# Optimization experiments

Measured on AMD Instinct MI355X. Metric: run time of the kernel, lower is better.

## Reference

```python
import jax, jax.numpy as jnp
import numpy as np

INPUT_DIM = 512
OUTPUT_DIM = 512
DEGREE = 7
ALPHA = 0.5


def setup_inputs() -> dict:
    key = jax.random.key(0)
    kx, kc = jax.random.split(key)
    x = jax.random.normal(kx, (8192, INPUT_DIM), dtype=jnp.float32)
    std = 1.0 / (INPUT_DIM * (DEGREE + 1))
    laguerre_coeffs = jax.random.normal(kc, (INPUT_DIM, OUTPUT_DIM, DEGREE + 1), dtype=jnp.float32) * std
    return {"x": x, "laguerre_coeffs": laguerre_coeffs}


def reference(x, laguerre_coeffs):
    # x: [B, I] -> tanh squashed
    xt = jnp.tanh(x.reshape(-1, INPUT_DIM))
    # Build Laguerre basis L_0..L_degree via the standard recurrence:
    # k*L_k = (2(k-1)+1+alpha - x)*L_{k-1} - (k-1+alpha)*L_{k-2}
    L0 = jnp.ones_like(xt)
    basis = [L0]
    if DEGREE > 0:
        L1 = 1.0 + ALPHA - xt
        basis.append(L1)
        Lkm2, Lkm1 = L0, L1
        for k in range(2, DEGREE + 1):
            Lk = ((2 * (k - 1) + 1 + ALPHA - xt) * Lkm1 - (k - 1 + ALPHA) * Lkm2) / k
            basis.append(Lk)
            Lkm2, Lkm1 = Lkm1, Lk
    laguerre = jnp.stack(basis, axis=-1)  # [B, I, D+1]
    y = jnp.einsum('bid,iod->bo', laguerre, laguerre_coeffs)
    return y
```

## Files before the change

### kernel.cpp

```cpp
#include <hip/hip_runtime.h>

#define B_ROWS 8192
#define IN_DIM 512
#define OUT_DIM 512
#define NDEG 8
#define KDIM (IN_DIM * NDEG)
#define ZSLICES 4
#define NKT 16

typedef short bf16x8 __attribute__((ext_vector_type(8)));
typedef float f32x4  __attribute__((ext_vector_type(4)));

__device__ __forceinline__ unsigned short f2bf(float f) {
  unsigned u = __float_as_uint(f);
  u += 0x7fffu + ((u >> 16) & 1u);
  return (unsigned short)(u >> 16);
}

__device__ __forceinline__ void laguerre8(float t, float* L) {
  L[0] = 1.0f;
  L[1] = 1.5f - t;
#pragma unroll
  for (int k = 2; k < NDEG; ++k)
    L[k] = ((2.0f * (float)k - 0.5f - t) * L[k - 1] -
            ((float)k - 0.5f) * L[k - 2]) * (1.0f / (float)k);
}


__global__ void prep_kernel(const float* __restrict__ x, const float* __restrict__ cf,
                            unsigned short* __restrict__ A, unsigned short* __restrict__ Bt) {
  int g = blockIdx.x;
  if (g < (B_ROWS * IN_DIM) / 256) {
    int idx = g * 256 + threadIdx.x;
    int b = idx >> 9, i = idx & 511;
    float L[NDEG];
    laguerre8(tanhf(x[idx]), L);
    uint4 v;
    v.x = (unsigned)f2bf(L[0]) | ((unsigned)f2bf(L[1]) << 16);
    v.y = (unsigned)f2bf(L[2]) | ((unsigned)f2bf(L[3]) << 16);
    v.z = (unsigned)f2bf(L[4]) | ((unsigned)f2bf(L[5]) << 16);
    v.w = (unsigned)f2bf(L[6]) | ((unsigned)f2bf(L[7]) << 16);
    int h = b >> 7, rb = b & 127, t = i >> 3, c = i & 7;
    size_t chunk = ((size_t)(h * 64 + t)) * 1024 + (rb >> 6) * 512 + (rb & 63) * 8 + (c ^ (rb & 7));
    ((uint4*)A)[chunk] = v;
  } else {
    int idx = (g - (B_ROWS * IN_DIM) / 256) * 256 + threadIdx.x;
    int i = idx >> 9, o = idx & 511;
    const float4* cp = (const float4*)(cf + (size_t)idx * 8);
    float4 c0 = cp[0], c1 = cp[1];
    uint4 v;
    v.x = (unsigned)f2bf(c0.x) | ((unsigned)f2bf(c0.y) << 16);
    v.y = (unsigned)f2bf(c0.z) | ((unsigned)f2bf(c0.w) << 16);
    v.z = (unsigned)f2bf(c1.x) | ((unsigned)f2bf(c1.y) << 16);
    v.w = (unsigned)f2bf(c1.z) | ((unsigned)f2bf(c1.w) << 16);
    int h = o >> 7, rb = o & 127, t = i >> 3, c = i & 7;
    size_t chunk = ((size_t)(h * 64 + t)) * 1024 + (rb >> 6) * 512 + (rb & 63) * 8 + (c ^ (rb & 7));
    ((uint4*)Bt)[chunk] = v;
  }
}

__global__ __launch_bounds__(512, 2) void gemm_kernel(const unsigned short* __restrict__ A,
                                                      const unsigned short* __restrict__ Bt,
                                                      unsigned short* __restrict__ P) {
  __shared__ unsigned short lds[65536];

  const int tid = threadIdx.x;
  const int lane = tid & 63;
  const int w = tid >> 6;
  const int wm = w >> 2, wn = w & 3;

  const int g = blockIdx.x;
  const int j0 = g >> 3, xx = g & 7;
  const int My = ((j0 >> 3) << 3) | xx;
  const int n = (j0 >> 2) & 1;
  const int z = j0 & 3;

  const uint4* Ag = (const uint4*)A;
  const uint4* Bg = (const uint4*)Bt;

  const int arow = lane & 15, hi = lane >> 4;
  const int e0 = (hi ^ (arow & 7)) * 8;

  f32x4 zero = {0.f, 0.f, 0.f, 0.f};
  f32x4 acc[8][4];
#pragma unroll
  for (int mi = 0; mi < 8; ++mi)
#pragma unroll
    for (int ni = 0; ni < 4; ++ni) acc[mi][ni] = zero;

  auto STAGE = [&](int tile, int buf) {
    const int tg = z * NKT + tile;
    const size_t cA0 = ((size_t)((My * 2 + 0) * 64 + tg)) * 1024 + w * 64 + lane;
    const size_t cA1 = ((size_t)((My * 2 + 1) * 64 + tg)) * 1024 + w * 64 + lane;
    const size_t cB0 = ((size_t)((n * 2 + 0) * 64 + tg)) * 1024 + w * 64 + lane;
    const size_t cB1 = ((size_t)((n * 2 + 1) * 64 + tg)) * 1024 + w * 64 + lane;
    unsigned short* dA = lds + buf * 16384 + w * 512;
    unsigned short* dB = lds + 32768 + buf * 16384 + w * 512;
#pragma unroll
    for (int j = 0; j < 2; ++j) {
      __builtin_amdgcn_global_load_lds(
          (const __attribute__((address_space(1))) unsigned int*)(Ag + cA0 + j * 512),
          (__attribute__((address_space(3))) unsigned int*)(dA + j * 4096), 16, 0, 0);
      __builtin_amdgcn_global_load_lds(
          (const __attribute__((address_space(1))) unsigned int*)(Ag + cA1 + j * 512),
          (__attribute__((address_space(3))) unsigned int*)(dA + 8192 + j * 4096), 16, 0, 0);
      __builtin_amdgcn_global_load_lds(
          (const __attribute__((address_space(1))) unsigned int*)(Bg + cB0 + j * 512),
          (__attribute__((address_space(3))) unsigned int*)(dB + j * 4096), 16, 0, 0);
      __builtin_amdgcn_global_load_lds(
          (const __attribute__((address_space(1))) unsigned int*)(Bg + cB1 + j * 512),
          (__attribute__((address_space(3))) unsigned int*)(dB + 8192 + j * 4096), 16, 0, 0);
    }
  };

  auto COMPUTE = [&](int buf) {
    const unsigned short* Ab = lds + buf * 16384 + wm * 8192;
    const unsigned short* Bb = lds + 32768 + buf * 16384 + (wn >> 1) * 8192 + (wn & 1) * 4096;
#pragma unroll
    for (int ks = 0; ks < 2; ++ks) {
      bf16x8 af[8], bfr[4];
#pragma unroll
      for (int mi = 0; mi < 8; ++mi)
        af[mi] = *(const bf16x8*)(Ab + (mi >> 2) * 4096 + ((mi & 3) * 16 + arow) * 64 + (e0 ^ (ks * 32)));
#pragma unroll
      for (int ni = 0; ni < 4; ++ni)
        bfr[ni] = *(const bf16x8*)(Bb + (ni * 16 + arow) * 64 + (e0 ^ (ks * 32)));
      __builtin_amdgcn_s_setprio(1);
#pragma unroll
      for (int mi = 0; mi < 8; ++mi)
#pragma unroll
        for (int ni = 0; ni < 4; ++ni)
          acc[mi][ni] = __builtin_amdgcn_mfma_f32_16x16x32_bf16(af[mi], bfr[ni], acc[mi][ni], 0, 0, 0);
      __builtin_amdgcn_s_setprio(0);
    }
  };

  STAGE(0, 0);
  STAGE(1, 1);
  asm volatile("s_waitcnt vmcnt(8)" ::: "memory");
  __builtin_amdgcn_sched_barrier(0);
  __builtin_amdgcn_s_barrier();

  for (int t = 0; t < NKT - 2; ++t) {
    const int cur = t & 1;
    COMPUTE(cur);
    asm volatile("s_waitcnt lgkmcnt(0)" ::: "memory");
    __builtin_amdgcn_sched_barrier(0);
    __builtin_amdgcn_s_barrier();
    STAGE(t + 2, cur);
    asm volatile("s_waitcnt vmcnt(8)" ::: "memory");
    __builtin_amdgcn_sched_barrier(0);
    __builtin_amdgcn_s_barrier();
  }
  COMPUTE(0);
  asm volatile("s_waitcnt vmcnt(0)" ::: "memory");
  __builtin_amdgcn_sched_barrier(0);
  __builtin_amdgcn_s_barrier();
  COMPUTE(1);
  __syncthreads();

  unsigned short* W = lds + w * 8192;
#pragma unroll
  for (int mi = 0; mi < 8; ++mi)
#pragma unroll
    for (int ni = 0; ni < 4; ++ni) {
      int col = ni * 16 + arow;
      int c8 = col >> 3, cpos = col & 7;
#pragma unroll
      for (int r = 0; r < 4; ++r) {
        int row = mi * 16 + hi * 4 + r;
        W[row * 64 + ((c8 ^ (row & 7)) << 3) + cpos] = f2bf(acc[mi][ni][r]);
      }
    }
  const int rr = lane >> 3, cc = lane & 7;
#pragma unroll
  for (int it = 0; it < 16; ++it) {
    int row = it * 8 + rr;
    uint4 v = *(uint4*)&W[row * 64 + ((cc ^ (row & 7)) << 3)];
    size_t pr = ((size_t)z * B_ROWS + My * 256 + wm * 128 + row) * 512 + n * 256 + wn * 64 + cc * 8;
    *(uint4*)&P[pr] = v;
  }
}

__global__ void reduce_kernel(const unsigned short* __restrict__ P, float* __restrict__ out) {
  size_t t = (size_t)blockIdx.x * 256 + threadIdx.x;
  const uint4* p = (const uint4*)P;
  const size_t stride = (size_t)B_ROWS * OUT_DIM / 8;
  float s[8] = {0, 0, 0, 0, 0, 0, 0, 0};
#pragma unroll
  for (int zz = 0; zz < ZSLICES; ++zz) {
    uint4 v = p[t + zz * stride];
    unsigned q[4] = {v.x, v.y, v.z, v.w};
#pragma unroll
    for (int j = 0; j < 4; ++j) {
      s[2 * j]     += __uint_as_float((q[j] & 0xffffu) << 16);
      s[2 * j + 1] += __uint_as_float(q[j] & 0xffff0000u);
    }
  }
  float4 o0 = {s[0], s[1], s[2], s[3]}, o1 = {s[4], s[5], s[6], s[7]};
  ((float4*)out)[t * 2]     = o0;
  ((float4*)out)[t * 2 + 1] = o1;
}

__global__ void naive_kernel(const float* __restrict__ x, const float* __restrict__ c,
                             float* __restrict__ out) {
  __shared__ float bas[IN_DIM * NDEG];
  int b = blockIdx.x;
  for (int i = threadIdx.x; i < IN_DIM; i += 256) {
    float t = tanhf(x[(size_t)b * IN_DIM + i]);
    float L[NDEG];
    laguerre8(t, L);
#pragma unroll
    for (int d = 0; d < NDEG; ++d) bas[i * NDEG + d] = L[d];
  }
  __syncthreads();
  for (int o = threadIdx.x; o < OUT_DIM; o += 256) {
    float acc = 0.f;
    for (int i = 0; i < IN_DIM; ++i) {
      const float* cp = c + ((size_t)i * OUT_DIM + o) * NDEG;
#pragma unroll
      for (int d = 0; d < NDEG; ++d) acc += bas[i * NDEG + d] * cp[d];
    }
    out[(size_t)b * OUT_DIM + o] = acc;
  }
}

extern "C" void kernel_launch(void* const* d_in, const int* in_sizes, int n_in,
                              void* d_out, int out_size, void* d_ws, size_t ws_size,
                              hipStream_t stream) {
  const float* x    = (const float*)d_in[0];
  const float* coef = (const float*)d_in[1];
  float* out = (float*)d_out;

  const size_t A_BYTES  = (size_t)B_ROWS * KDIM * 2;
  const size_t P_BYTES  = (size_t)ZSLICES * B_ROWS * OUT_DIM * 2;
  const size_t BT_BYTES = (size_t)OUT_DIM * KDIM * 2;

  if (ws_size >= A_BYTES + P_BYTES + BT_BYTES) {
    unsigned short* Abuf = (unsigned short*)d_ws;
    unsigned short* Pp   = (unsigned short*)((char*)d_ws + A_BYTES);
    unsigned short* Bt   = (unsigned short*)((char*)d_ws + A_BYTES + P_BYTES);
    prep_kernel<<<(B_ROWS * IN_DIM + IN_DIM * OUT_DIM) / 256, 256, 0, stream>>>(x, coef, Abuf, Bt);
    gemm_kernel<<<256, 512, 0, stream>>>(Abuf, Bt, Pp);
    reduce_kernel<<<(B_ROWS * OUT_DIM / 8) / 256, 256, 0, stream>>>(Pp, out);
  } else {
    naive_kernel<<<B_ROWS, 256, 0, stream>>>(x, coef, out);
  }
}
```

Before: 67.95 us.

## Interleave half-tile async loads with MFMA phases in fine-grained GEMM pipeline

Replaces the per-tile compute-then-stage double-buffer loop with eight phases per tile pair, each issuing one half-tile global-to-LDS load and running a quarter of the MFMA work, with barriers and vmcnt waits placed between phases. Fragment registers shrink to 4 A and 4 B vectors. The aim is to spread memory traffic across compute so loads overlap MFMA execution more evenly and register pressure drops. The cost is many more barriers per tile and tighter ordering assumptions about which buffer halves are safe to overwrite.

```diff
diff --git a/kernel.cpp b/kernel.cpp
--- a/kernel.cpp
+++ b/kernel.cpp
@@ -59,6 +59,35 @@
   }
 }
 
+
+#define PH(buf, mq, ks, LOADBF, VMW, ...)                                          \
+  {                                                                                \
+    const unsigned short* Ab_ = lds + (buf)*16384 + wm*8192 + (mq)*4096 + arow*64; \
+    _Pragma("unroll") for (int m4 = 0; m4 < 4; ++m4)                               \
+      af[m4] = *(const bf16x8*)(Ab_ + m4*1024 + (e ^ ((ks)*32)));                  \
+    if (LOADBF) {                                                                  \
+      const unsigned short* Bb_ = lds + 32768 + (buf)*16384 + (wn>>1)*8192         \
+                                  + (wn&1)*4096 + arow*64;                         \
+      _Pragma("unroll") for (int ni = 0; ni < 4; ++ni)                             \
+        bfr[ni] = *(const bf16x8*)(Bb_ + ni*1024 + (e ^ ((ks)*32)));               \
+    }                                                                              \
+    __VA_ARGS__;                                                                   \
+    __builtin_amdgcn_s_barrier();                                                  \
+    asm volatile("s_waitcnt lgkmcnt(0)" ::: "memory");                             \
+    __builtin_amdgcn_sched_barrier(0);                                             \
+    __builtin_amdgcn_s_setprio(1);                                                 \
+    _Pragma("unroll") for (int m4 = 0; m4 < 4; ++m4)                               \
+      _Pragma("unroll") for (int ni = 0; ni < 4; ++ni)                             \
+        acc[(mq)*4+m4][ni] = __builtin_amdgcn_mfma_f32_16x16x32_bf16(              \
+            af[m4], bfr[ni], acc[(mq)*4+m4][ni], 0, 0, 0);                         \
+    __builtin_amdgcn_s_setprio(0);                                                 \
+    if ((VMW) == 1) { asm volatile("s_waitcnt vmcnt(2)" ::: "memory");             \
+                      __builtin_amdgcn_sched_barrier(0); }                         \
+    if ((VMW) == 2) { asm volatile("s_waitcnt vmcnt(0)" ::: "memory");             \
+                      __builtin_amdgcn_sched_barrier(0); }                         \
+    __builtin_amdgcn_s_barrier();                                                  \
+  }
+
 __global__ __launch_bounds__(512, 2) void gemm_kernel(const unsigned short* __restrict__ A,
                                                       const unsigned short* __restrict__ Bt,
                                                       unsigned short* __restrict__ P) {
@@ -79,7 +108,7 @@
   const uint4* Bg = (const uint4*)Bt;
 
   const int arow = lane & 15, hi = lane >> 4;
-  const int e0 = (hi ^ (arow & 7)) * 8;
+  const int e = (hi ^ (arow & 7)) * 8;
 
   f32x4 zero = {0.f, 0.f, 0.f, 0.f};
   f32x4 acc[8][4];
@@ -88,76 +117,47 @@
 #pragma unroll
     for (int ni = 0; ni < 4; ++ni) acc[mi][ni] = zero;
 
-  auto STAGE = [&](int tile, int buf) {
-    const int tg = z * NKT + tile;
-    const size_t cA0 = ((size_t)((My * 2 + 0) * 64 + tg)) * 1024 + w * 64 + lane;
-    const size_t cA1 = ((size_t)((My * 2 + 1) * 64 + tg)) * 1024 + w * 64 + lane;
-    const size_t cB0 = ((size_t)((n * 2 + 0) * 64 + tg)) * 1024 + w * 64 + lane;
-    const size_t cB1 = ((size_t)((n * 2 + 1) * 64 + tg)) * 1024 + w * 64 + lane;
-    unsigned short* dA = lds + buf * 16384 + w * 512;
-    unsigned short* dB = lds + 32768 + buf * 16384 + w * 512;
-#pragma unroll
-    for (int j = 0; j < 2; ++j) {
-      __builtin_amdgcn_global_load_lds(
-          (const __attribute__((address_space(1))) unsigned int*)(Ag + cA0 + j * 512),
-          (__attribute__((address_space(3))) unsigned int*)(dA + j * 4096), 16, 0, 0);
-      __builtin_amdgcn_global_load_lds(
-          (const __attribute__((address_space(1))) unsigned int*)(Ag + cA1 + j * 512),
-          (__attribute__((address_space(3))) unsigned int*)(dA + 8192 + j * 4096), 16, 0, 0);
-      __builtin_amdgcn_global_load_lds(
-          (const __attribute__((address_space(1))) unsigned int*)(Bg + cB0 + j * 512),
-          (__attribute__((address_space(3))) unsigned int*)(dB + j * 4096), 16, 0, 0);
-      __builtin_amdgcn_global_load_lds(
-          (const __attribute__((address_space(1))) unsigned int*)(Bg + cB1 + j * 512),
-          (__attribute__((address_space(3))) unsigned int*)(dB + 8192 + j * 4096), 16, 0, 0);
-    }
+  auto STAGE_H = [&](int isB, int h, int tile, int buf) {
+    const uint4* src = isB ? Bg : Ag;
+    const int rowblk = (isB ? n * 2 : My * 2) + h;
+    const size_t c0 = ((size_t)(rowblk * 64 + z * NKT + tile)) * 1024 + w * 64 + lane;
+    unsigned short* d = lds + isB * 32768 + buf * 16384 + h * 8192 + w * 512;
+    __builtin_amdgcn_global_load_lds(
+        (const __attribute__((address_space(1))) unsigned int*)(src + c0),
+        (__attribute__((address_space(3))) unsigned int*)d, 16, 0, 0);
+    __builtin_amdgcn_global_load_lds(
+        (const __attribute__((address_space(1))) unsigned int*)(src + c0 + 512),
+        (__attribute__((address_space(3))) unsigned int*)(d + 4096), 16, 0, 0);
   };
 
-  auto COMPUTE = [&](int buf) {
-    const unsigned short* Ab = lds + buf * 16384 + wm * 8192;
-    const unsigned short* Bb = lds + 32768 + buf * 16384 + (wn >> 1) * 8192 + (wn & 1) * 4096;
-#pragma unroll
-    for (int ks = 0; ks < 2; ++ks) {
-      bf16x8 af[8], bfr[4];
-#pragma unroll
-      for (int mi = 0; mi < 8; ++mi)
-        af[mi] = *(const bf16x8*)(Ab + (mi >> 2) * 4096 + ((mi & 3) * 16 + arow) * 64 + (e0 ^ (ks * 32)));
-#pragma unroll
-      for (int ni = 0; ni < 4; ++ni)
-        bfr[ni] = *(const bf16x8*)(Bb + (ni * 16 + arow) * 64 + (e0 ^ (ks * 32)));
-      __builtin_amdgcn_s_setprio(1);
-#pragma unroll
-      for (int mi = 0; mi < 8; ++mi)
-#pragma unroll
-        for (int ni = 0; ni < 4; ++ni)
-          acc[mi][ni] = __builtin_amdgcn_mfma_f32_16x16x32_bf16(af[mi], bfr[ni], acc[mi][ni], 0, 0, 0);
-      __builtin_amdgcn_s_setprio(0);
-    }
-  };
-
-  STAGE(0, 0);
-  STAGE(1, 1);
-  asm volatile("s_waitcnt vmcnt(8)" ::: "memory");
+  bf16x8 af[4], bfr[4];
+
+  STAGE_H(0, 0, 0, 0); STAGE_H(0, 1, 0, 0);
+  STAGE_H(1, 0, 0, 0); STAGE_H(1, 1, 0, 0);
+  STAGE_H(1, 0, 1, 1);
+  asm volatile("s_waitcnt vmcnt(2)" ::: "memory");
   __builtin_amdgcn_sched_barrier(0);
   __builtin_amdgcn_s_barrier();
 
-  for (int t = 0; t < NKT - 2; ++t) {
-    const int cur = t & 1;
-    COMPUTE(cur);
-    asm volatile("s_waitcnt lgkmcnt(0)" ::: "memory");
-    __builtin_amdgcn_sched_barrier(0);
-    __builtin_amdgcn_s_barrier();
-    STAGE(t + 2, cur);
-    asm volatile("s_waitcnt vmcnt(8)" ::: "memory");
-    __builtin_amdgcn_sched_barrier(0);
-    __builtin_amdgcn_s_barrier();
-  }
-  COMPUTE(0);
-  asm volatile("s_waitcnt vmcnt(0)" ::: "memory");
-  __builtin_amdgcn_sched_barrier(0);
-  __builtin_amdgcn_s_barrier();
-  COMPUTE(1);
-  __syncthreads();
+  for (int it = 0; it < 7; ++it) {
+    const int t1 = 2 * it + 1, t2 = 2 * it + 2, t3 = 2 * it + 3;
+    PH(0, 0, 0, 1, 0, STAGE_H(1, 1, t1, 1));
+    PH(0, 1, 0, 0, 0, STAGE_H(0, 0, t1, 1));
+    PH(0, 0, 1, 1, 0, STAGE_H(0, 1, t1, 1));
+    PH(0, 1, 1, 0, 1, STAGE_H(1, 0, t2, 0));
+    PH(1, 0, 0, 1, 0, STAGE_H(0, 0, t2, 0));
+    PH(1, 1, 0, 0, 0, STAGE_H(0, 1, t2, 0));
+    PH(1, 0, 1, 1, 0, STAGE_H(1, 1, t2, 0));
+    PH(1, 1, 1, 0, 1, STAGE_H(1, 0, t3, 1));
+  }
+  PH(0, 0, 0, 1, 0, STAGE_H(1, 1, 15, 1));
+  PH(0, 1, 0, 0, 0, STAGE_H(0, 0, 15, 1));
+  PH(0, 0, 1, 1, 0, STAGE_H(0, 1, 15, 1));
+  PH(0, 1, 1, 0, 2, (void)0);
+  PH(1, 0, 0, 1, 0, (void)0);
+  PH(1, 1, 0, 0, 0, (void)0);
+  PH(1, 0, 1, 1, 0, (void)0);
+  PH(1, 1, 1, 0, 0, (void)0);
 
   unsigned short* W = lds + w * 8192;
 #pragma unroll
```

New measurement: 67.10 us. About the same (-1.2%).

## Fuse split-K reduction into GEMM via atomic counters and shrink tiles

Applied to the files above, without the earlier changes.

Tiles shrink from 256x256 to 128x128 with split-K reduced from 4 to 2 slices, so 512 blocks run with 4 blocks per CU and smaller LDS. The separate reduce kernel is removed: the last block per output tile, found with an atomic counter, sums the two bf16 partials into the output. The prep kernel now writes contiguous swizzled A chunks with coalesced stores and uses a fast exp-based tanh. This cuts one kernel launch and halves partial-sum traffic, at the cost of a memset, atomics and lower per-block reuse.

```diff
diff --git a/kernel.cpp b/kernel.cpp
--- a/kernel.cpp
+++ b/kernel.cpp
@@ -5,8 +5,8 @@
 #define OUT_DIM 512
 #define NDEG 8
 #define KDIM (IN_DIM * NDEG)
-#define ZSLICES 4
-#define NKT 16
+#define ZS 2
+#define NKT 32
 
 typedef short bf16x8 __attribute__((ext_vector_type(8)));
 typedef float f32x4  __attribute__((ext_vector_type(4)));
@@ -26,25 +26,39 @@
             ((float)k - 0.5f) * L[k - 2]) * (1.0f / (float)k);
 }
 
+__device__ __forceinline__ float ftanh(float x) {
+  float e2 = __expf(2.0f * x);
+  return (e2 - 1.0f) * (1.0f / (e2 + 1.0f));
+}
+
+__device__ __forceinline__ uint4 bpack(float xv) {
+  float L[NDEG];
+  laguerre8(ftanh(xv), L);
+  uint4 v;
+  v.x = (unsigned)f2bf(L[0]) | ((unsigned)f2bf(L[1]) << 16);
+  v.y = (unsigned)f2bf(L[2]) | ((unsigned)f2bf(L[3]) << 16);
+  v.z = (unsigned)f2bf(L[4]) | ((unsigned)f2bf(L[5]) << 16);
+  v.w = (unsigned)f2bf(L[6]) | ((unsigned)f2bf(L[7]) << 16);
+  return v;
+}
+
 
 __global__ void prep_kernel(const float* __restrict__ x, const float* __restrict__ cf,
                             unsigned short* __restrict__ A, unsigned short* __restrict__ Bt) {
-  int g = blockIdx.x;
-  if (g < (B_ROWS * IN_DIM) / 256) {
-    int idx = g * 256 + threadIdx.x;
-    int b = idx >> 9, i = idx & 511;
-    float L[NDEG];
-    laguerre8(tanhf(x[idx]), L);
-    uint4 v;
-    v.x = (unsigned)f2bf(L[0]) | ((unsigned)f2bf(L[1]) << 16);
-    v.y = (unsigned)f2bf(L[2]) | ((unsigned)f2bf(L[3]) << 16);
-    v.z = (unsigned)f2bf(L[4]) | ((unsigned)f2bf(L[5]) << 16);
-    v.w = (unsigned)f2bf(L[6]) | ((unsigned)f2bf(L[7]) << 16);
-    int h = b >> 7, rb = b & 127, t = i >> 3, c = i & 7;
-    size_t chunk = ((size_t)(h * 64 + t)) * 1024 + (rb >> 6) * 512 + (rb & 63) * 8 + (c ^ (rb & 7));
-    ((uint4*)A)[chunk] = v;
+  const int g = blockIdx.x, tid = threadIdx.x;
+  if (g < 4096) {
+    const int h = g >> 6, t = g & 63;
+    uint4* dst = (uint4*)A + (size_t)g * 1024;
+#pragma unroll
+    for (int q = 0; q < 4; ++q) {
+      int v = q * 256 + tid;
+      int rb = ((v >> 9) << 6) | ((v >> 3) & 63);
+      int c = (v & 7) ^ (rb & 7);
+      float xv = x[(size_t)(h * 128 + rb) * 512 + t * 8 + c];
+      dst[v] = bpack(xv);
+    }
   } else {
-    int idx = (g - (B_ROWS * IN_DIM) / 256) * 256 + threadIdx.x;
+    int idx = (g - 4096) * 256 + tid;
     int i = idx >> 9, o = idx & 511;
     const float4* cp = (const float4*)(cf + (size_t)idx * 8);
     float4 c0 = cp[0], c1 = cp[1];
@@ -59,10 +73,21 @@
   }
 }
 
-__global__ __launch_bounds__(512, 2) void gemm_kernel(const unsigned short* __restrict__ A,
+
+#define VM(N) { asm volatile("s_waitcnt vmcnt(" #N ")" ::: "memory");  \
+                __builtin_amdgcn_sched_barrier(0); }
+#define GL16(s, d)                                                      \
+  __builtin_amdgcn_global_load_lds(                                     \
+      (const __attribute__((address_space(1))) unsigned int*)(s),       \
+      (__attribute__((address_space(3))) unsigned int*)(d), 16, 0, 0)
+
+__global__ __launch_bounds__(512, 4) void gemm_kernel(const unsigned short* __restrict__ A,
                                                       const unsigned short* __restrict__ Bt,
-                                                      unsigned short* __restrict__ P) {
-  __shared__ unsigned short lds[65536];
+                                                      unsigned short* __restrict__ P,
+                                                      float* __restrict__ out,
+                                                      unsigned int* __restrict__ cnt) {
+  __shared__ __align__(16) unsigned short lds[32768];
+  __shared__ int lastFlag;
 
   const int tid = threadIdx.x;
   const int lane = tid & 63;
@@ -70,77 +95,61 @@
   const int wm = w >> 2, wn = w & 3;
 
   const int g = blockIdx.x;
-  const int j0 = g >> 3, xx = g & 7;
-  const int My = ((j0 >> 3) << 3) | xx;
-  const int n = (j0 >> 2) & 1;
-  const int z = j0 & 3;
+  const int slot = g >> 3, xcd = g & 7;
+  const int My = ((slot & 7) << 3) | xcd;
+  const int n = (slot >> 3) & 3;
+  const int z = slot >> 5;
 
   const uint4* Ag = (const uint4*)A;
   const uint4* Bg = (const uint4*)Bt;
 
   const int arow = lane & 15, hi = lane >> 4;
-  const int e0 = (hi ^ (arow & 7)) * 8;
+  const int e = (hi ^ (arow & 7)) * 8;
 
   f32x4 zero = {0.f, 0.f, 0.f, 0.f};
-  f32x4 acc[8][4];
-#pragma unroll
-  for (int mi = 0; mi < 8; ++mi)
-#pragma unroll
-    for (int ni = 0; ni < 4; ++ni) acc[mi][ni] = zero;
-
-  auto STAGE = [&](int tile, int buf) {
-    const int tg = z * NKT + tile;
-    const size_t cA0 = ((size_t)((My * 2 + 0) * 64 + tg)) * 1024 + w * 64 + lane;
-    const size_t cA1 = ((size_t)((My * 2 + 1) * 64 + tg)) * 1024 + w * 64 + lane;
-    const size_t cB0 = ((size_t)((n * 2 + 0) * 64 + tg)) * 1024 + w * 64 + lane;
-    const size_t cB1 = ((size_t)((n * 2 + 1) * 64 + tg)) * 1024 + w * 64 + lane;
-    unsigned short* dA = lds + buf * 16384 + w * 512;
-    unsigned short* dB = lds + 32768 + buf * 16384 + w * 512;
-#pragma unroll
-    for (int j = 0; j < 2; ++j) {
-      __builtin_amdgcn_global_load_lds(
-          (const __attribute__((address_space(1))) unsigned int*)(Ag + cA0 + j * 512),
-          (__attribute__((address_space(3))) unsigned int*)(dA + j * 4096), 16, 0, 0);
-      __builtin_amdgcn_global_load_lds(
-          (const __attribute__((address_space(1))) unsigned int*)(Ag + cA1 + j * 512),
-          (__attribute__((address_space(3))) unsigned int*)(dA + 8192 + j * 4096), 16, 0, 0);
-      __builtin_amdgcn_global_load_lds(
-          (const __attribute__((address_space(1))) unsigned int*)(Bg + cB0 + j * 512),
-          (__attribute__((address_space(3))) unsigned int*)(dB + j * 4096), 16, 0, 0);
-      __builtin_amdgcn_global_load_lds(
-          (const __attribute__((address_space(1))) unsigned int*)(Bg + cB1 + j * 512),
-          (__attribute__((address_space(3))) unsigned int*)(dB + 8192 + j * 4096), 16, 0, 0);
-    }
+  f32x4 acc[4][2];
+#pragma unroll
+  for (int m4 = 0; m4 < 4; ++m4)
+#pragma unroll
+    for (int ni = 0; ni < 2; ++ni) acc[m4][ni] = zero;
+
+  auto STAGE = [&](int t, int buf) {
+    const int tg = z * NKT + t;
+    const uint4* a = Ag + ((size_t)(My * 64 + tg)) * 1024 + w * 128 + lane;
+    unsigned short* dA = lds + buf * 8192 + w * 1024;
+    GL16(a, dA); GL16(a + 64, dA + 512);
+    const uint4* b = Bg + ((size_t)(n * 64 + tg)) * 1024 + w * 128 + lane;
+    unsigned short* dB = lds + 16384 + buf * 8192 + w * 1024;
+    GL16(b, dB); GL16(b + 64, dB + 512);
   };
 
   auto COMPUTE = [&](int buf) {
-    const unsigned short* Ab = lds + buf * 16384 + wm * 8192;
-    const unsigned short* Bb = lds + 32768 + buf * 16384 + (wn >> 1) * 8192 + (wn & 1) * 4096;
+    const unsigned short* Ab = lds + buf * 8192 + wm * 4096 + arow * 64;
+    const unsigned short* Bb = lds + 16384 + buf * 8192 + (wn >> 1) * 4096
+                               + (wn & 1) * 2048 + arow * 64;
 #pragma unroll
     for (int ks = 0; ks < 2; ++ks) {
-      bf16x8 af[8], bfr[4];
-#pragma unroll
-      for (int mi = 0; mi < 8; ++mi)
-        af[mi] = *(const bf16x8*)(Ab + (mi >> 2) * 4096 + ((mi & 3) * 16 + arow) * 64 + (e0 ^ (ks * 32)));
-#pragma unroll
-      for (int ni = 0; ni < 4; ++ni)
-        bfr[ni] = *(const bf16x8*)(Bb + (ni * 16 + arow) * 64 + (e0 ^ (ks * 32)));
+      const int o = e ^ (ks * 32);
+      bf16x8 af[4], bfr[2];
+#pragma unroll
+      for (int m4 = 0; m4 < 4; ++m4) af[m4] = *(const bf16x8*)(Ab + m4 * 1024 + o);
+#pragma unroll
+      for (int ni = 0; ni < 2; ++ni) bfr[ni] = *(const bf16x8*)(Bb + ni * 1024 + o);
       __builtin_amdgcn_s_setprio(1);
 #pragma unroll
-      for (int mi = 0; mi < 8; ++mi)
-#pragma unroll
-        for (int ni = 0; ni < 4; ++ni)
-          acc[mi][ni] = __builtin_amdgcn_mfma_f32_16x16x32_bf16(af[mi], bfr[ni], acc[mi][ni], 0, 0, 0);
+      for (int m4 = 0; m4 < 4; ++m4)
+#pragma unroll
+        for (int ni = 0; ni < 2; ++ni)
+          acc[m4][ni] = __builtin_amdgcn_mfma_f32_16x16x32_bf16(af[m4], bfr[ni], acc[m4][ni], 0, 0, 0);
       __builtin_amdgcn_s_setprio(0);
     }
   };
 
-  STAGE(0, 0);
-  STAGE(1, 1);
-  asm volatile("s_waitcnt vmcnt(8)" ::: "memory");
-  __builtin_amdgcn_sched_barrier(0);
+  STAGE(0, 0); STAGE(1, 1);
+  VM(4);
   __builtin_amdgcn_s_barrier();
 
+#pragma unroll 2
   for (int t = 0; t < NKT - 2; ++t) {
     const int cur = t & 1;
     COMPUTE(cur);
@@ -148,58 +157,65 @@
     __builtin_amdgcn_sched_barrier(0);
     __builtin_amdgcn_s_barrier();
     STAGE(t + 2, cur);
-    asm volatile("s_waitcnt vmcnt(8)" ::: "memory");
-    __builtin_amdgcn_sched_barrier(0);
+    VM(4);
     __builtin_amdgcn_s_barrier();
   }
   COMPUTE(0);
-  asm volatile("s_waitcnt vmcnt(0)" ::: "memory");
-  __builtin_amdgcn_sched_barrier(0);
+  VM(0);
   __builtin_amdgcn_s_barrier();
   COMPUTE(1);
   __syncthreads();
 
-  unsigned short* W = lds + w * 8192;
-#pragma unroll
-  for (int mi = 0; mi < 8; ++mi)
-#pragma unroll
-    for (int ni = 0; ni < 4; ++ni) {
+  unsigned short* W = lds + w * 4096;
+#pragma unroll
+  for (int m4 = 0; m4 < 4; ++m4)
+#pragma unroll
+    for (int ni = 0; ni < 2; ++ni) {
       int col = ni * 16 + arow;
       int c8 = col >> 3, cpos = col & 7;
 #pragma unroll
       for (int r = 0; r < 4; ++r) {
-        int row = mi * 16 + hi * 4 + r;
-        W[row * 64 + ((c8 ^ (row & 7)) << 3) + cpos] = f2bf(acc[mi][ni][r]);
+        int row = m4 * 16 + hi * 4 + r;
+        W[row * 64 + ((c8 ^ (row & 7)) << 3) + cpos] = f2bf(acc[m4][ni][r]);
       }
     }
-  const int rr = lane >> 3, cc = lane & 7;
-#pragma unroll
-  for (int it = 0; it < 16; ++it) {
-    int row = it * 8 + rr;
-    uint4 v = *(uint4*)&W[row * 64 + ((cc ^ (row & 7)) << 3)];
-    size_t pr = ((size_t)z * B_ROWS + My * 256 + wm * 128 + row) * 512 + n * 256 + wn * 64 + cc * 8;
+#pragma unroll
+  for (int it = 0; it < 4; ++it) {
+    int row = it * 16 + (lane >> 2), cc2 = lane & 3;
+    uint4 v = *(uint4*)&W[row * 64 + ((cc2 ^ (row & 7)) << 3)];
+    size_t pr = (size_t)z * ((size_t)B_ROWS * OUT_DIM)
+              + (size_t)(My * 128 + wm * 64 + row) * 512 + n * 128 + wn * 32 + cc2 * 8;
     *(uint4*)&P[pr] = v;
   }
-}
-
-__global__ void reduce_kernel(const unsigned short* __restrict__ P, float* __restrict__ out) {
-  size_t t = (size_t)blockIdx.x * 256 + threadIdx.x;
-  const uint4* p = (const uint4*)P;
-  const size_t stride = (size_t)B_ROWS * OUT_DIM / 8;
-  float s[8] = {0, 0, 0, 0, 0, 0, 0, 0};
-#pragma unroll
-  for (int zz = 0; zz < ZSLICES; ++zz) {
-    uint4 v = p[t + zz * stride];
-    unsigned q[4] = {v.x, v.y, v.z, v.w};
-#pragma unroll
-    for (int j = 0; j < 4; ++j) {
-      s[2 * j]     += __uint_as_float((q[j] & 0xffffu) << 16);
-      s[2 * j + 1] += __uint_as_float(q[j] & 0xffff0000u);
-    }
-  }
-  float4 o0 = {s[0], s[1], s[2], s[3]}, o1 = {s[4], s[5], s[6], s[7]};
-  ((float4*)out)[t * 2]     = o0;
-  ((float4*)out)[t * 2 + 1] = o1;
+
+  __threadfence();
+  if (tid == 0)
+    lastFlag = (atomicAdd(&cnt[My * 4 + n], 1u) == 1u);
+  __syncthreads();
+  if (lastFlag) {
+    __threadfence();
+    const size_t ss = (size_t)B_ROWS * OUT_DIM;
+#pragma unroll
+    for (int q = 0; q < 4; ++q) {
+      int el = q * 512 + tid;
+      int row = el >> 4, cc = el & 15;
+      size_t off = (size_t)(My * 128 + row) * 512 + n * 128 + cc * 8;
+      uint4 a = *(const uint4*)&P[off];
+      uint4 b = *(const uint4*)&P[off + ss];
+      unsigned qa[4] = {a.x, a.y, a.z, a.w}, qb[4] = {b.x, b.y, b.z, b.w};
+      float s[8];
+#pragma unroll
+      for (int j = 0; j < 4; ++j) {
+        s[2 * j]     = __uint_as_float((qa[j] & 0xffffu) << 16) +
+                       __uint_as_float((qb[j] & 0xffffu) << 16);
+        s[2 * j + 1] = __uint_as_float(qa[j] & 0xffff0000u) +
+                       __uint_as_float(qb[j] & 0xffff0000u);
+      }
+      float4 f0 = {s[0], s[1], s[2], s[3]}, f1 = {s[4], s[5], s[6], s[7]};
+      *(float4*)&out[off]     = f0;
+      *(float4*)&out[off + 4] = f1;
+    }
+  }
 }
 
 __global__ void naive_kernel(const float* __restrict__ x, const float* __restrict__ c,
@@ -232,17 +248,19 @@
   const float* coef = (const float*)d_in[1];
   float* out = (float*)d_out;
 
-  const size_t A_BYTES  = (size_t)B_ROWS * KDIM * 2;
-  const size_t P_BYTES  = (size_t)ZSLICES * B_ROWS * OUT_DIM * 2;
-  const size_t BT_BYTES = (size_t)OUT_DIM * KDIM * 2;
-
-  if (ws_size >= A_BYTES + P_BYTES + BT_BYTES) {
+  const size_t A_B   = (size_t)B_ROWS * KDIM * 2;
+  const size_t P_B   = (size_t)ZS * B_ROWS * OUT_DIM * 2;
+  const size_t BT_B  = (size_t)OUT_DIM * KDIM * 2;
+  const size_t CNT_B = 1024;
+
+  if (ws_size >= A_B + P_B + BT_B + CNT_B) {
     unsigned short* Abuf = (unsigned short*)d_ws;
-    unsigned short* Pp   = (unsigned short*)((char*)d_ws + A_BYTES);
-    unsigned short* Bt   = (unsigned short*)((char*)d_ws + A_BYTES + P_BYTES);
-    prep_kernel<<<(B_ROWS * IN_DIM + IN_DIM * OUT_DIM) / 256, 256, 0, stream>>>(x, coef, Abuf, Bt);
-    gemm_kernel<<<256, 512, 0, stream>>>(Abuf, Bt, Pp);
-    reduce_kernel<<<(B_ROWS * OUT_DIM / 8) / 256, 256, 0, stream>>>(Pp, out);
+    unsigned short* Pp   = (unsigned short*)((char*)d_ws + A_B);
+    unsigned short* Bt   = (unsigned short*)((char*)d_ws + A_B + P_B);
+    unsigned int*   cnt  = (unsigned int*)((char*)d_ws + A_B + P_B + BT_B);
+    hipMemsetAsync(cnt, 0, CNT_B, stream);
+    prep_kernel<<<4096 + 1024, 256, 0, stream>>>(x, coef, Abuf, Bt);
+    gemm_kernel<<<512, 512, 0, stream>>>(Abuf, Bt, Pp, out, cnt);
   } else {
     naive_kernel<<<B_ROWS, 256, 0, stream>>>(x, coef, out);
   }
```

Result: slower. 239.6 us (+252.6%).

## Shrink GEMM tiles to 128x128, halve split-K slices, use fast tanh

Applied to the files above, without the earlier changes.

The GEMM block tile goes from 256x256 with 8 waves to 128x128 with 4 waves, and the launch goes from 256 to 512 blocks. Split-K drops from 4 slices to 2, so each block runs 32 K-tiles and the partial buffer and reduce traffic are halved. The prep kernel swaps tanhf for an exp-based fast tanh, which is cheaper but could overflow for large inputs. Smaller tiles mean less data reuse per block and more global traffic for A and B, in exchange for fewer partial sums and possibly better occupancy; s_setprio is also dropped.

```diff
diff --git a/kernel.cpp b/kernel.cpp
--- a/kernel.cpp
+++ b/kernel.cpp
@@ -5,11 +5,13 @@
 #define OUT_DIM 512
 #define NDEG 8
 #define KDIM (IN_DIM * NDEG)
-#define ZSLICES 4
-#define NKT 16
+#define ZS 2
+#define NKT 32
 
 typedef short bf16x8 __attribute__((ext_vector_type(8)));
 typedef float f32x4  __attribute__((ext_vector_type(4)));
+
+#define SB __builtin_amdgcn_sched_barrier(0)
 
 __device__ __forceinline__ unsigned short f2bf(float f) {
   unsigned u = __float_as_uint(f);
@@ -24,6 +26,22 @@
   for (int k = 2; k < NDEG; ++k)
     L[k] = ((2.0f * (float)k - 0.5f - t) * L[k - 1] -
             ((float)k - 0.5f) * L[k - 2]) * (1.0f / (float)k);
+}
+
+__device__ __forceinline__ float ftanh(float x) {
+  float e2 = __expf(2.0f * x);
+  return (e2 - 1.0f) * (1.0f / (e2 + 1.0f));
+}
+
+__device__ __forceinline__ uint4 bpack(float xv) {
+  float L[NDEG];
+  laguerre8(ftanh(xv), L);
+  uint4 v;
+  v.x = (unsigned)f2bf(L[0]) | ((unsigned)f2bf(L[1]) << 16);
+  v.y = (unsigned)f2bf(L[2]) | ((unsigned)f2bf(L[3]) << 16);
+  v.z = (unsigned)f2bf(L[4]) | ((unsigned)f2bf(L[5]) << 16);
+  v.w = (unsigned)f2bf(L[6]) | ((unsigned)f2bf(L[7]) << 16);
+  return v;
 }
 
 
@@ -33,13 +51,7 @@
   if (g < (B_ROWS * IN_DIM) / 256) {
     int idx = g * 256 + threadIdx.x;
     int b = idx >> 9, i = idx & 511;
-    float L[NDEG];
-    laguerre8(tanhf(x[idx]), L);
-    uint4 v;
-    v.x = (unsigned)f2bf(L[0]) | ((unsigned)f2bf(L[1]) << 16);
-    v.y = (unsigned)f2bf(L[2]) | ((unsigned)f2bf(L[3]) << 16);
-    v.z = (unsigned)f2bf(L[4]) | ((unsigned)f2bf(L[5]) << 16);
-    v.w = (unsigned)f2bf(L[6]) | ((unsigned)f2bf(L[7]) << 16);
+    uint4 v = bpack(x[idx]);
     int h = b >> 7, rb = b & 127, t = i >> 3, c = i & 7;
     size_t chunk = ((size_t)(h * 64 + t)) * 1024 + (rb >> 6) * 512 + (rb & 63) * 8 + (c ^ (rb & 7));
     ((uint4*)A)[chunk] = v;
@@ -59,109 +71,97 @@
   }
 }
 
-__global__ __launch_bounds__(512, 2) void gemm_kernel(const unsigned short* __restrict__ A,
+__global__ __launch_bounds__(256, 2) void gemm_kernel(const unsigned short* __restrict__ A,
                                                       const unsigned short* __restrict__ Bt,
                                                       unsigned short* __restrict__ P) {
-  __shared__ unsigned short lds[65536];
+  __shared__ unsigned short lds[32768];
 
   const int tid = threadIdx.x;
   const int lane = tid & 63;
   const int w = tid >> 6;
-  const int wm = w >> 2, wn = w & 3;
+  const int wm = w >> 1, wn = w & 1;
 
   const int g = blockIdx.x;
-  const int j0 = g >> 3, xx = g & 7;
-  const int My = ((j0 >> 3) << 3) | xx;
-  const int n = (j0 >> 2) & 1;
-  const int z = j0 & 3;
+  const int xx = g & 7, hy = (g >> 3) & 7;
+  const int My = hy * 8 + xx;
+  const int n = (g >> 6) & 3;
+  const int z = (g >> 8) & 1;
 
   const uint4* Ag = (const uint4*)A;
   const uint4* Bg = (const uint4*)Bt;
 
   const int arow = lane & 15, hi = lane >> 4;
-  const int e0 = (hi ^ (arow & 7)) * 8;
+  const int e = (hi ^ (arow & 7)) * 8;
 
   f32x4 zero = {0.f, 0.f, 0.f, 0.f};
-  f32x4 acc[8][4];
-#pragma unroll
-  for (int mi = 0; mi < 8; ++mi)
+  f32x4 acc[4][4];
+#pragma unroll
+  for (int mi = 0; mi < 4; ++mi)
 #pragma unroll
     for (int ni = 0; ni < 4; ++ni) acc[mi][ni] = zero;
 
   auto STAGE = [&](int tile, int buf) {
     const int tg = z * NKT + tile;
-    const size_t cA0 = ((size_t)((My * 2 + 0) * 64 + tg)) * 1024 + w * 64 + lane;
-    const size_t cA1 = ((size_t)((My * 2 + 1) * 64 + tg)) * 1024 + w * 64 + lane;
-    const size_t cB0 = ((size_t)((n * 2 + 0) * 64 + tg)) * 1024 + w * 64 + lane;
-    const size_t cB1 = ((size_t)((n * 2 + 1) * 64 + tg)) * 1024 + w * 64 + lane;
-    unsigned short* dA = lds + buf * 16384 + w * 512;
-    unsigned short* dB = lds + 32768 + buf * 16384 + w * 512;
-#pragma unroll
-    for (int j = 0; j < 2; ++j) {
+    const size_t cA = ((size_t)(My * 64 + tg)) * 1024 + w * 256 + lane;
+    const size_t cB = ((size_t)(n * 64 + tg)) * 1024 + w * 256 + lane;
+    unsigned short* dA = lds + buf * 8192 + w * 2048;
+    unsigned short* dB = lds + 16384 + buf * 8192 + w * 2048;
+#pragma unroll
+    for (int j = 0; j < 4; ++j) {
       __builtin_amdgcn_global_load_lds(
-          (const __attribute__((address_space(1))) unsigned int*)(Ag + cA0 + j * 512),
-          (__attribute__((address_space(3))) unsigned int*)(dA + j * 4096), 16, 0, 0);
+          (const __attribute__((address_space(1))) unsigned int*)(Ag + cA + j * 64),
+          (__attribute__((address_space(3))) unsigned int*)(dA + j * 512), 16, 0, 0);
       __builtin_amdgcn_global_load_lds(
-          (const __attribute__((address_space(1))) unsigned int*)(Ag + cA1 + j * 512),
-          (__attribute__((address_space(3))) unsigned int*)(dA + 8192 + j * 4096), 16, 0, 0);
-      __builtin_amdgcn_global_load_lds(
-          (const __attribute__((address_space(1))) unsigned int*)(Bg + cB0 + j * 512),
-          (__attribute__((address_space(3))) unsigned int*)(dB + j * 4096), 16, 0, 0);
-      __builtin_amdgcn_global_load_lds(
-          (const __attribute__((address_space(1))) unsigned int*)(Bg + cB1 + j * 512),
-          (__attribute__((address_space(3))) unsigned int*)(dB + 8192 + j * 4096), 16, 0, 0);
+          (const __attribute__((address_space(1))) unsigned int*)(Bg + cB + j * 64),
+          (__attribute__((address_space(3))) unsigned int*)(dB + j * 512), 16, 0, 0);
     }
   };
 
   auto COMPUTE = [&](int buf) {
-    const unsigned short* Ab = lds + buf * 16384 + wm * 8192;
-    const unsigned short* Bb = lds + 32768 + buf * 16384 + (wn >> 1) * 8192 + (wn & 1) * 4096;
+    const unsigned short* Ab = lds + buf * 8192 + wm * 4096 + arow * 64;
+    const unsigned short* Bb = lds + 16384 + buf * 8192 + wn * 4096 + arow * 64;
 #pragma unroll
     for (int ks = 0; ks < 2; ++ks) {
-      bf16x8 af[8], bfr[4];
-#pragma unroll
-      for (int mi = 0; mi < 8; ++mi)
-        af[mi] = *(const bf16x8*)(Ab + (mi >> 2) * 4096 + ((mi & 3) * 16 + arow) * 64 + (e0 ^ (ks * 32)));
-#pragma unroll
-      for (int ni = 0; ni < 4; ++ni)
-        bfr[ni] = *(const bf16x8*)(Bb + (ni * 16 + arow) * 64 + (e0 ^ (ks * 32)));
-      __builtin_amdgcn_s_setprio(1);
-#pragma unroll
-      for (int mi = 0; mi < 8; ++mi)
+      const int o = e ^ (ks * 32);
+      bf16x8 af[4], bfr[4];
+#pragma unroll
+      for (int m4 = 0; m4 < 4; ++m4) af[m4] = *(const bf16x8*)(Ab + m4 * 1024 + o);
+#pragma unroll
+      for (int ni = 0; ni < 4; ++ni) bfr[ni] = *(const bf16x8*)(Bb + ni * 1024 + o);
+#pragma unroll
+      for (int m4 = 0; m4 < 4; ++m4)
 #pragma unroll
         for (int ni = 0; ni < 4; ++ni)
-          acc[mi][ni] = __builtin_amdgcn_mfma_f32_16x16x32_bf16(af[mi], bfr[ni], acc[mi][ni], 0, 0, 0);
-      __builtin_amdgcn_s_setprio(0);
+          acc[m4][ni] = __builtin_amdgcn_mfma_f32_16x16x32_bf16(af[m4], bfr[ni], acc[m4][ni], 0, 0, 0);
     }
   };
 
-  STAGE(0, 0);
-  STAGE(1, 1);
+  STAGE(0, 0); STAGE(1, 1);
   asm volatile("s_waitcnt vmcnt(8)" ::: "memory");
-  __builtin_amdgcn_sched_barrier(0);
-  __builtin_amdgcn_s_barrier();
+  SB;
+  __builtin_amdgcn_s_barrier(); SB;
 
   for (int t = 0; t < NKT - 2; ++t) {
     const int cur = t & 1;
     COMPUTE(cur);
     asm volatile("s_waitcnt lgkmcnt(0)" ::: "memory");
-    __builtin_amdgcn_sched_barrier(0);
-    __builtin_amdgcn_s_barrier();
+    SB;
+    __builtin_amdgcn_s_barrier(); SB;
     STAGE(t + 2, cur);
     asm volatile("s_waitcnt vmcnt(8)" ::: "memory");
-    __builtin_amdgcn_sched_barrier(0);
-    __builtin_amdgcn_s_barrier();
+    SB;
+    __builtin_amdgcn_s_barrier(); SB;
   }
   COMPUTE(0);
   asm volatile("s_waitcnt vmcnt(0)" ::: "memory");
-  __builtin_amdgcn_sched_barrier(0);
-  __builtin_amdgcn_s_barrier();
+  SB;
+  __builtin_amdgcn_s_barrier(); SB;
   COMPUTE(1);
   __syncthreads();
 
   unsigned short* W = lds + w * 8192;
 #pragma unroll
-  for (int mi = 0; mi < 8; ++mi)
+  for (int mi = 0; mi < 4; ++mi)
 #pragma unroll
     for (int ni = 0; ni < 4; ++ni) {
       int col = ni * 16 + arow;
@@ -174,10 +174,10 @@
     }
   const int rr = lane >> 3, cc = lane & 7;
 #pragma unroll
-  for (int it = 0; it < 16; ++it) {
+  for (int it = 0; it < 8; ++it) {
     int row = it * 8 + rr;
     uint4 v = *(uint4*)&W[row * 64 + ((cc ^ (row & 7)) << 3)];
-    size_t pr = ((size_t)z * B_ROWS + My * 256 + wm * 128 + row) * 512 + n * 256 + wn * 64 + cc * 8;
+    size_t pr = ((size_t)z * B_ROWS + My * 128 + wm * 64 + row) * 512 + n * 128 + wn * 64 + cc * 8;
     *(uint4*)&P[pr] = v;
   }
 }
@@ -188,7 +188,7 @@
   const size_t stride = (size_t)B_ROWS * OUT_DIM / 8;
   float s[8] = {0, 0, 0, 0, 0, 0, 0, 0};
 #pragma unroll
-  for (int zz = 0; zz < ZSLICES; ++zz) {
+  for (int zz = 0; zz < ZS; ++zz) {
     uint4 v = p[t + zz * stride];
     unsigned q[4] = {v.x, v.y, v.z, v.w};
 #pragma unroll
@@ -207,9 +207,8 @@
   __shared__ float bas[IN_DIM * NDEG];
   int b = blockIdx.x;
   for (int i = threadIdx.x; i < IN_DIM; i += 256) {
-    float t = tanhf(x[(size_t)b * IN_DIM + i]);
     float L[NDEG];
-    laguerre8(t, L);
+    laguerre8(tanhf(x[(size_t)b * IN_DIM + i]), L);
 #pragma unroll
     for (int d = 0; d < NDEG; ++d) bas[i * NDEG + d] = L[d];
   }
@@ -232,16 +231,16 @@
   const float* coef = (const float*)d_in[1];
   float* out = (float*)d_out;
 
-  const size_t A_BYTES  = (size_t)B_ROWS * KDIM * 2;
-  const size_t P_BYTES  = (size_t)ZSLICES * B_ROWS * OUT_DIM * 2;
-  const size_t BT_BYTES = (size_t)OUT_DIM * KDIM * 2;
-
-  if (ws_size >= A_BYTES + P_BYTES + BT_BYTES) {
+  const size_t A_B  = (size_t)B_ROWS * KDIM * 2;
+  const size_t P_B  = (size_t)ZS * B_ROWS * OUT_DIM * 2;
+  const size_t BT_B = (size_t)OUT_DIM * KDIM * 2;
+
+  if (ws_size >= A_B + P_B + BT_B) {
     unsigned short* Abuf = (unsigned short*)d_ws;
-    unsigned short* Pp   = (unsigned short*)((char*)d_ws + A_BYTES);
-    unsigned short* Bt   = (unsigned short*)((char*)d_ws + A_BYTES + P_BYTES);
-    prep_kernel<<<(B_ROWS * IN_DIM + IN_DIM * OUT_DIM) / 256, 256, 0, stream>>>(x, coef, Abuf, Bt);
-    gemm_kernel<<<256, 512, 0, stream>>>(Abuf, Bt, Pp);
+    unsigned short* Pp   = (unsigned short*)((char*)d_ws + A_B);
+    unsigned short* Bt   = (unsigned short*)((char*)d_ws + A_B + P_B);
+    prep_kernel<<<(B_ROWS * IN_DIM) / 256 + (IN_DIM * OUT_DIM) / 256, 256, 0, stream>>>(x, coef, Abuf, Bt);
+    gemm_kernel<<<512, 256, 0, stream>>>(Abuf, Bt, Pp);
     reduce_kernel<<<(B_ROWS * OUT_DIM / 8) / 256, 256, 0, stream>>>(Pp, out);
   } else {
     naive_kernel<<<B_ROWS, 256, 0, stream>>>(x, coef, out);
```

Measured after the change: 66.78 us. Within noise of the previous version (-1.7%).
